# Kernel tuning notes

Measured on AMD Instinct MI355X. Metric: run time of the kernel, lower is better.

## Reference

```python
import jax, jax.numpy as jnp
import numpy as np
import math

C_Z, C_HID, N_HEADS = 128, 32, 4
B, N = 1, 320
LN_EPS = 1e-5


def setup_inputs() -> dict:
    key = jax.random.key(0)
    ks = jax.random.split(key, 9)
    d = C_HID * N_HEADS  # 128
    glorot = math.sqrt(2.0 / (C_Z + d))
    return {
        "z": jax.random.normal(ks[0], (B, N, N, C_Z), jnp.float32),
        "mask_bias": jax.random.normal(ks[1], (B, N, 1, 1, N), jnp.float32),
        "edge_bias": jax.random.normal(ks[2], (B, 1, N_HEADS, N, N), jnp.float32),
        "wq": jax.random.normal(ks[3], (d, C_Z), jnp.float32) * glorot,
        "wk": jax.random.normal(ks[4], (d, C_Z), jnp.float32) * glorot,
        "wv": jax.random.normal(ks[5], (d, C_Z), jnp.float32) * glorot,
        "wg": jax.random.normal(ks[6], (d, C_Z), jnp.float32) * 0.02,
        "wo": jax.random.normal(ks[7], (C_Z, d), jnp.float32) * 0.02,
        "ln_w": jnp.ones((C_Z,), jnp.float32),
        "ln_b": jnp.zeros((C_Z,), jnp.float32),
    }


def reference(z, mask_bias, edge_bias, wq, wk, wv, wg, wo, ln_w, ln_b):
    # LayerNorm over c_z
    mu = jnp.mean(z, axis=-1, keepdims=True)
    var = jnp.mean(jnp.square(z - mu), axis=-1, keepdims=True)
    zn = (z - mu) * jax.lax.rsqrt(var + LN_EPS) * ln_w + ln_b  # [B,I,J,c_z]

    def proj(w):
        p = jnp.einsum("bijd,ed->bije", zn, w)  # [B,I,J,H*c]
        p = p.reshape(zn.shape[:-1] + (N_HEADS, C_HID))  # [B,I,J,H,c]
        return jnp.swapaxes(p, -3, -2)  # [B,I,H,J,c]

    q = proj(wq) / math.sqrt(C_HID)
    k = proj(wk)
    v = proj(wv)

    # scores: [B,I,H,Q,K] + mask_bias [B,I,1,1,K] + edge_bias [B,1,H,Q,K]
    scores = jnp.einsum("bihqc,bihkc->bihqk", q, k) + mask_bias + edge_bias
    a = jax.nn.softmax(scores, axis=-1)
    o = jnp.einsum("bihqk,bihkc->bihqc", a, v)  # [B,I,H,J,c]
    o = jnp.swapaxes(o, -3, -2)  # [B,I,J,H,c]

    g = jax.nn.sigmoid(jnp.einsum("bijd,ed->bije", zn, wg))
    g = g.reshape(zn.shape[:-1] + (N_HEADS, C_HID))
    o = o * g

    o = o.reshape(o.shape[:-2] + (N_HEADS * C_HID,))  # [B,I,J,H*c]
    return jnp.einsum("bije,de->bijd", o, wo)  # [B,I,J,c_z]
```

## Files before the change

### kernel.cpp

```cpp
#include <hip/hip_runtime.h>
#include <hip/hip_bf16.h>

#define NRES 320
#define CZ 128
#define NH 4
#define CH 32
#define DM 128
#define NPOS (NRES*NRES)
#define LN_EPS 1e-5f
#define QSCALE 0.17677669529663687f
#define LOG2E 1.4426950408889634f

using bf16 = __hip_bfloat16;
typedef __attribute__((ext_vector_type(8))) short short8;
typedef __attribute__((ext_vector_type(4))) float floatx4;

__device__ __forceinline__ float bflo(uint32_t u){ return __uint_as_float(u << 16); }
__device__ __forceinline__ float bfhi(uint32_t u){ return __uint_as_float(u & 0xffff0000u); }
__device__ __forceinline__ bf16 tob(float f){ return __float2bfloat16(f); }
__device__ __forceinline__ uint32_t cvtpk(float a, float b){
    uint32_t r;
    asm("v_cvt_pk_bf16_f32 %0, %1, %2" : "=v"(r) : "v"(a), "v"(b));
    return r;
}

__global__ __launch_bounds__(256)
void k_packw(const float* __restrict__ wq, const float* __restrict__ wk,
             const float* __restrict__ wv, const float* __restrict__ wg,
             bf16* __restrict__ Apkh, bf16* __restrict__ Apkl)
{
    const int idx = blockIdx.x * 256 + threadIdx.x;
    const int j = idx & 7, lane = (idx >> 3) & 63;
    const int ks = (idx >> 9) & 3, mf = (idx >> 11) & 3, wid = idx >> 13;
    const int e = wid*64 + mf*16 + (lane & 15);
    const int k = ks*32 + (lane >> 4)*8 + j;
    const float* w = (e >> 7) == 0 ? wq : (e >> 7) == 1 ? wk : (e >> 7) == 2 ? wv : wg;
    float wv_ = w[(e & 127)*CZ + k];
    if (e < 128) wv_ *= QSCALE * LOG2E;
    const bf16 hb = tob(wv_);
    Apkh[idx] = hb;
    Apkl[idx] = tob(wv_ - __bfloat162float(hb));
}

__global__ __launch_bounds__(256)
void k_packwo(const float* __restrict__ wo, bf16* __restrict__ B2h,
              bf16* __restrict__ B2l)
{
    const int idx = blockIdx.x * 256 + threadIdx.x;
    const int j = idx & 7, lane = (idx >> 3) & 63;
    const int nr = (idx >> 9) & 3, ks = (idx >> 11) & 3, wn = idx >> 13;
    const int n = wn*64 + nr*16 + (lane & 15);
    const int k = ks*32 + ((lane >> 4) << 3) + j;
    const float wv_ = wo[n*DM + k];
    const bf16 hb = tob(wv_);
    B2h[idx] = hb;
    B2l[idx] = tob(wv_ - __bfloat162float(hb));
}

__global__ __launch_bounds__(256)
void k_packeb(const float* __restrict__ eb, bf16* __restrict__ ebpk)
{
    const int idx = blockIdx.x * 256 + threadIdx.x;
    const int e = idx & 7;
    const int lane = (idx >> 3) & 63;
    const int nf = (idx >> 9) & 3;
    const int w = (idx >> 11) % 5;
    const int t = (idx / 10240) % 10;
    const int h = idx / 102400;
    const int q = w*64 + nf*16 + (lane & 15);
    const int k = t*32 + (e >> 2)*16 + (lane >> 4)*4 + (e & 3);
    ebpk[idx] = tob(eb[((size_t)h*NRES + q)*NRES + k] * LOG2E);
}

__global__ __launch_bounds__(256)
void k_packmb(const float* __restrict__ mb, float* __restrict__ mbpk)
{
    const int idx = blockIdx.x * 256 + threadIdx.x;
    mbpk[idx] = mb[idx] * LOG2E;
}

__global__ __launch_bounds__(512, 3)
void k_lnproj(const float* __restrict__ z, const float* __restrict__ ln_w,
              const float* __restrict__ ln_b, const bf16* __restrict__ Apkh,
              const bf16* __restrict__ Apkl,
              bf16* __restrict__ qws, bf16* __restrict__ kws,
              bf16* __restrict__ vtws, bf16* __restrict__ gows)
{
    __shared__ __align__(16) char Bsh[16 * 1040];
    __shared__ __align__(16) char Bsl[16 * 1040];
    const int tid = threadIdx.x;
    const int p0 = blockIdx.x * 64;
    const int lane = tid & 63, wid = tid >> 6;
    const int l15 = lane & 15, g = lane >> 4;

    {
        const int r = tid >> 3, t = tid & 7, c0 = t*16;
        const float* zp = z + (size_t)(p0 + r)*CZ + c0;
        float v[16];
        {
            float4 t0 = *(const float4*)(zp + 0);
            float4 t1 = *(const float4*)(zp + 4);
            float4 t2 = *(const float4*)(zp + 8);
            float4 t3 = *(const float4*)(zp + 12);
            v[0]=t0.x; v[1]=t0.y; v[2]=t0.z; v[3]=t0.w;
            v[4]=t1.x; v[5]=t1.y; v[6]=t1.z; v[7]=t1.w;
            v[8]=t2.x; v[9]=t2.y; v[10]=t2.z; v[11]=t2.w;
            v[12]=t3.x; v[13]=t3.y; v[14]=t3.z; v[15]=t3.w;
        }
        float s = 0.f, s2 = 0.f;
        #pragma unroll
        for (int c = 0; c < 16; ++c) { s += v[c]; s2 = fmaf(v[c], v[c], s2); }
        s  += __shfl_xor(s, 1);  s  += __shfl_xor(s, 2);  s  += __shfl_xor(s, 4);
        s2 += __shfl_xor(s2, 1); s2 += __shfl_xor(s2, 2); s2 += __shfl_xor(s2, 4);
        const float mu = s * 0.0078125f;
        const float rs = rsqrtf(s2 * 0.0078125f - mu*mu + LN_EPS);
        float vn[16];
        #pragma unroll
        for (int c = 0; c < 16; ++c)
            vn[c] = (v[c] - mu) * rs * ln_w[c0 + c] + ln_b[c0 + c];
        uint32_t hd[8], ld[8];
        #pragma unroll
        for (int c2 = 0; c2 < 8; ++c2) {
            hd[c2] = cvtpk(vn[2*c2], vn[2*c2+1]);
            ld[c2] = cvtpk(vn[2*c2]   - bflo(hd[c2]),
                           vn[2*c2+1] - bfhi(hd[c2]));
        }
        *(uint4*)(Bsh + (2*t    )*1040 + r*16) = make_uint4(hd[0], hd[1], hd[2], hd[3]);
        *(uint4*)(Bsh + (2*t + 1)*1040 + r*16) = make_uint4(hd[4], hd[5], hd[6], hd[7]);
        *(uint4*)(Bsl + (2*t    )*1040 + r*16) = make_uint4(ld[0], ld[1], ld[2], ld[3]);
        *(uint4*)(Bsl + (2*t + 1)*1040 + r*16) = make_uint4(ld[4], ld[5], ld[6], ld[7]);
    }
    __syncthreads();

    floatx4 acc[4][4];
    #pragma unroll
    for (int mf = 0; mf < 4; ++mf)
        #pragma unroll
        for (int nf = 0; nf < 4; ++nf)
            acc[mf][nf] = (floatx4){0.f, 0.f, 0.f, 0.f};

    const uint4* aph = (const uint4*)Apkh;
    const uint4* apl = (const uint4*)Apkl;
    #pragma unroll
    for (int ks = 0; ks < 4; ++ks) {
        uint4 ahv[4], alv[4];
        #pragma unroll
        for (int mf = 0; mf < 4; ++mf) {
            ahv[mf] = aph[((wid*4 + mf)*4 + ks)*64 + lane];
            alv[mf] = apl[((wid*4 + mf)*4 + ks)*64 + lane];
        }
        #pragma unroll
        for (int nf = 0; nf < 4; ++nf) {
            const int off = (ks*4 + g)*1040 + (16*nf + l15)*16;
            const short8 bh = *(const short8*)(Bsh + off);
            const short8 bl = *(const short8*)(Bsl + off);
            #pragma unroll
            for (int mf = 0; mf < 4; ++mf) {
                const short8 ah = *(const short8*)&ahv[mf];
                const short8 al = *(const short8*)&alv[mf];
                acc[mf][nf] = __builtin_amdgcn_mfma_f32_16x16x32_bf16(ah, bh, acc[mf][nf], 0, 0, 0);
                acc[mf][nf] = __builtin_amdgcn_mfma_f32_16x16x32_bf16(al, bh, acc[mf][nf], 0, 0, 0);
                acc[mf][nf] = __builtin_amdgcn_mfma_f32_16x16x32_bf16(ah, bl, acc[mf][nf], 0, 0, 0);
            }
        }
    }

    const int i = p0 / NRES;
    const int j0 = p0 % NRES;
    #pragma unroll
    for (int mf = 0; mf < 4; ++mf) {
        const int e0 = wid*64 + mf*16 + 4*g;
        const int hh = (e0 >> 5) & 3, c0 = e0 & 31;
        #pragma unroll
        for (int nf = 0; nf < 4; ++nf) {
            const int jl = nf*16 + l15;
            const floatx4 a = acc[mf][nf];
            if (wid < 4) {
                uint2 dw;
                dw.x = cvtpk(a[0], a[1]);
                dw.y = cvtpk(a[2], a[3]);
                bf16* dst = (wid < 2) ? qws : kws;
                const size_t hidx = ((size_t)((i*NH + hh)*NRES) + (j0 + jl))*CH + c0;
                *(uint2*)(dst + hidx) = dw;
            } else if (wid < 6) {
                const size_t vbase = ((size_t)((i*NH + hh)*CH) + c0)*NRES + (j0 + jl);
                vtws[vbase         ] = tob(a[0]);
                vtws[vbase +   NRES] = tob(a[1]);
                vtws[vbase + 2*NRES] = tob(a[2]);
                vtws[vbase + 3*NRES] = tob(a[3]);
            } else {
                const float g0 = 1.f / (1.f + __expf(-a[0]));
                const float g1 = 1.f / (1.f + __expf(-a[1]));
                const float g2 = 1.f / (1.f + __expf(-a[2]));
                const float g3 = 1.f / (1.f + __expf(-a[3]));
                uint2 dw;
                dw.x = cvtpk(g0, g1);
                dw.y = cvtpk(g2, g3);
                *(uint2*)(gows + (size_t)(p0 + jl)*DM + (e0 & 127)) = dw;
            }
        }
    }
}

__global__ __launch_bounds__(320, 3)
void k_attn(const bf16* __restrict__ qws, const bf16* __restrict__ kws,
            const bf16* __restrict__ vtws, bf16* __restrict__ gows,
            const float* __restrict__ mbpk, const bf16* __restrict__ ebpk)
{
    __shared__ __align__(16) char psmem[5 * 64 * 80];
    const int i = blockIdx.x, h = blockIdx.y;
    const int tid = threadIdx.x;
    const int lane = tid & 63, w = tid >> 6;
    const int l15 = lane & 15, g = lane >> 4;
    const size_t slab = (size_t)(i*NH + h) * NRES * CH;
    char* psb = psmem + w*5120;

    const uint4* qg = (const uint4*)(qws + slab);
    const uint4* kg = (const uint4*)(kws + slab);
    const uint4* vg = (const uint4*)(vtws + slab);
    const float* mbr = mbpk + (size_t)i*NRES;
    const uint4* ebp = (const uint4*)ebpk;
    const int ebbase = h*12800 + w*256 + lane;

    short8 bq[4];
    #pragma unroll
    for (int nf = 0; nf < 4; ++nf) {
        uint4 t = qg[(64*w + 16*nf + l15)*4 + g];
        bq[nf] = *(short8*)&t;
    }
    uint4 kc0 = kg[(     l15)*4 + g];
    uint4 kc1 = kg[(16 + l15)*4 + g];
    uint4 ebc[4];
    #pragma unroll
    for (int nf = 0; nf < 4; ++nf) ebc[nf] = ebp[ebbase + nf*64];

    floatx4 o[2][4];
    #pragma unroll
    for (int ma = 0; ma < 2; ++ma)
        #pragma unroll
        for (int nf = 0; nf < 4; ++nf)
            o[ma][nf] = (floatx4){0.f, 0.f, 0.f, 0.f};
    float m[4] = {-1e30f, -1e30f, -1e30f, -1e30f};
    float l[4] = {0.f, 0.f, 0.f, 0.f};

    for (int t = 0; t < 10; ++t) {
        uint4 av0u = vg[(     l15)*40 + 4*t + g];
        uint4 av1u = vg[(16 + l15)*40 + 4*t + g];
        float2 mbv[2][2];
        #pragma unroll
        for (int mi = 0; mi < 2; ++mi)
            #pragma unroll
            for (int rp = 0; rp < 2; ++rp)
                mbv[mi][rp] = *(const float2*)(mbr + 32*t + 16*mi + 4*g + 2*rp);

        const short8 ak0 = *(short8*)&kc0;
        const short8 ak1 = *(short8*)&kc1;
        floatx4 sa[2][4];
        #pragma unroll
        for (int nf = 0; nf < 4; ++nf) {
            sa[0][nf] = __builtin_amdgcn_mfma_f32_16x16x32_bf16(ak0, bq[nf], (floatx4){0.f,0.f,0.f,0.f}, 0, 0, 0);
            sa[1][nf] = __builtin_amdgcn_mfma_f32_16x16x32_bf16(ak1, bq[nf], (floatx4){0.f,0.f,0.f,0.f}, 0, 0, 0);
        }
        const int tn = (t < 9) ? t + 1 : 9;
        uint4 kn0 = kg[(32*tn +      l15)*4 + g];
        uint4 kn1 = kg[(32*tn + 16 + l15)*4 + g];
        uint4 ebn[4];
        #pragma unroll
        for (int nf = 0; nf < 4; ++nf) ebn[nf] = ebp[ebbase + tn*1280 + nf*64];

        float sv[4][2][4];
        float lmax[4];
        #pragma unroll
        for (int nf = 0; nf < 4; ++nf) {
            const uint4 E = ebc[nf];
            sv[nf][0][0] = sa[0][nf][0] + (bflo(E.x) + mbv[0][0].x);
            sv[nf][0][1] = sa[0][nf][1] + (bfhi(E.x) + mbv[0][0].y);
            sv[nf][0][2] = sa[0][nf][2] + (bflo(E.y) + mbv[0][1].x);
            sv[nf][0][3] = sa[0][nf][3] + (bfhi(E.y) + mbv[0][1].y);
            sv[nf][1][0] = sa[1][nf][0] + (bflo(E.z) + mbv[1][0].x);
            sv[nf][1][1] = sa[1][nf][1] + (bfhi(E.z) + mbv[1][0].y);
            sv[nf][1][2] = sa[1][nf][2] + (bflo(E.w) + mbv[1][1].x);
            sv[nf][1][3] = sa[1][nf][3] + (bfhi(E.w) + mbv[1][1].y);
            const float a0 = fmaxf(fmaxf(sv[nf][0][0], sv[nf][0][1]), fmaxf(sv[nf][0][2], sv[nf][0][3]));
            const float a1 = fmaxf(fmaxf(sv[nf][1][0], sv[nf][1][1]), fmaxf(sv[nf][1][2], sv[nf][1][3]));
            lmax[nf] = fmaxf(a0, a1);
        }
        const float gm = fmaxf(fmaxf(lmax[0] - m[0], lmax[1] - m[1]),
                               fmaxf(lmax[2] - m[2], lmax[3] - m[3]));
        if (__any(gm > 12.0f)) {
            #pragma unroll
            for (int nf = 0; nf < 4; ++nf) {
                float pm = lmax[nf];
                pm = fmaxf(pm, __shfl_xor(pm, 16));
                pm = fmaxf(pm, __shfl_xor(pm, 32));
                const float mn = fmaxf(m[nf], pm);
                const float sc = exp2f(m[nf] - mn);
                l[nf] *= sc;
                #pragma unroll
                for (int ma = 0; ma < 2; ++ma)
                    #pragma unroll
                    for (int r = 0; r < 4; ++r)
                        o[ma][nf][r] *= sc;
                m[nf] = mn;
            }
        }
        #pragma unroll
        for (int nf = 0; nf < 4; ++nf) {
            const int qrow = 16*nf + l15;
            #pragma unroll
            for (int mi = 0; mi < 2; ++mi) {
                const float p0 = exp2f(sv[nf][mi][0] - m[nf]);
                const float p1 = exp2f(sv[nf][mi][1] - m[nf]);
                const float p2 = exp2f(sv[nf][mi][2] - m[nf]);
                const float p3 = exp2f(sv[nf][mi][3] - m[nf]);
                l[nf] += (p0 + p1) + (p2 + p3);
                *(uint2*)(psb + qrow*80 + 32*mi + 8*g) =
                    make_uint2(cvtpk(p0, p1), cvtpk(p2, p3));
            }
        }
        const short8 av0 = *(short8*)&av0u;
        const short8 av1 = *(short8*)&av1u;
        #pragma unroll
        for (int nf = 0; nf < 4; ++nf) {
            const short8 bp = *(const short8*)(psb + (16*nf + l15)*80 + 16*g);
            o[0][nf] = __builtin_amdgcn_mfma_f32_16x16x32_bf16(av0, bp, o[0][nf], 0, 0, 0);
            o[1][nf] = __builtin_amdgcn_mfma_f32_16x16x32_bf16(av1, bp, o[1][nf], 0, 0, 0);
        }
        kc0 = kn0; kc1 = kn1;
        #pragma unroll
        for (int nf = 0; nf < 4; ++nf) ebc[nf] = ebn[nf];
    }

    float linv[4];
    #pragma unroll
    for (int nf = 0; nf < 4; ++nf) {
        float ls = l[nf];
        ls += __shfl_xor(ls, 16);
        ls += __shfl_xor(ls, 32);
        linv[nf] = 1.f / ls;
    }
    uint32_t* gp = (uint32_t*)gows;
    #pragma unroll
    for (int nf = 0; nf < 4; ++nf) {
        const int jq = 64*w + 16*nf + l15;
        #pragma unroll
        for (int ma = 0; ma < 2; ++ma)
            #pragma unroll
            for (int rp = 0; rp < 2; ++rp) {
                const size_t idx = ((size_t)(i*NRES + jq))*64 + h*16 + 8*ma + 2*g + rp;
                const uint32_t u = gp[idx];
                const float v0 = o[ma][nf][2*rp    ] * linv[nf] * bflo(u);
                const float v1 = o[ma][nf][2*rp + 1] * linv[nf] * bfhi(u);
                gp[idx] = cvtpk(v0, v1);
            }
    }
}

__global__ __launch_bounds__(512)
void k_outproj(const bf16* __restrict__ gows, const bf16* __restrict__ B2h,
               const bf16* __restrict__ B2l, float* __restrict__ out)
{
    __shared__ __align__(16) char As[16 * 4112];
    const int tid = threadIdx.x;
    const int p0 = blockIdx.x * 256;
    const int lane = tid & 63, wid = tid >> 6;
    const int wm = wid >> 1, wn = wid & 1;

    short8 bh[4][4];
    {
        const uint4* bp = (const uint4*)B2h;
        #pragma unroll
        for (int ks = 0; ks < 4; ++ks)
            #pragma unroll
            for (int nr = 0; nr < 4; ++nr) {
                uint4 t = bp[(((wn*4 + ks)*4) + nr)*64 + lane];
                bh[ks][nr] = *(short8*)&t;
            }
    }

    {
        const uint4* src = (const uint4*)(gows + (size_t)p0 * DM);
        #pragma unroll
        for (int it = 0; it < 8; ++it) {
            const int t = tid + it*512;
            uint4 u = src[t];
            *(uint4*)(As + (t & 15)*4112 + (t >> 4)*16) = u;
        }
    }
    __syncthreads();

    floatx4 acc[4][4];
    #pragma unroll
    for (int m = 0; m < 4; ++m)
        #pragma unroll
        for (int n = 0; n < 4; ++n)
            acc[m][n] = (floatx4){0.f, 0.f, 0.f, 0.f};

    const uint4* bpl = (const uint4*)B2l;
    #pragma unroll
    for (int ks = 0; ks < 4; ++ks) {
        short8 a[4];
        #pragma unroll
        for (int m = 0; m < 4; ++m) {
            const int row = wm*64 + m*16 + (lane & 15);
            a[m] = *(const short8*)(As + (ks*4 + (lane >> 4))*4112 + row*16);
        }
        #pragma unroll
        for (int nr = 0; nr < 4; ++nr) {
            uint4 tl = bpl[(((wn*4 + ks)*4) + nr)*64 + lane];
            const short8 bl = *(short8*)&tl;
            #pragma unroll
            for (int m = 0; m < 4; ++m)
                acc[m][nr] = __builtin_amdgcn_mfma_f32_16x16x32_bf16(a[m], bh[ks][nr], acc[m][nr], 0, 0, 0);
            #pragma unroll
            for (int m = 0; m < 4; ++m)
                acc[m][nr] = __builtin_amdgcn_mfma_f32_16x16x32_bf16(a[m], bl, acc[m][nr], 0, 0, 0);
        }
    }

    #pragma unroll
    for (int m = 0; m < 4; ++m) {
        #pragma unroll
        for (int n = 0; n < 4; ++n) {
            const int d = wn*64 + n*16 + (lane & 15);
            #pragma unroll
            for (int r = 0; r < 4; ++r) {
                const int prow = p0 + wm*64 + m*16 + ((lane >> 4) << 2) + r;
                out[(size_t)prow*DM + d] = acc[m][n][r];
            }
        }
    }
}

extern "C" void kernel_launch(void* const* d_in, const int* in_sizes, int n_in,
                              void* d_out, int out_size, void* d_ws, size_t ws_size,
                              hipStream_t stream)
{
    const float* z   = (const float*)d_in[0];
    const float* mb  = (const float*)d_in[1];
    const float* eb  = (const float*)d_in[2];
    const float* wq  = (const float*)d_in[3];
    const float* wk  = (const float*)d_in[4];
    const float* wv  = (const float*)d_in[5];
    const float* wg  = (const float*)d_in[6];
    const float* wo  = (const float*)d_in[7];
    const float* lnw = (const float*)d_in[8];
    const float* lnb = (const float*)d_in[9];
    float* out = (float*)d_out;

    const size_t SEG = (size_t)NPOS * DM;
    bf16* qws  = (bf16*)d_ws;
    bf16* kws  = qws + SEG;
    bf16* vtws = kws + SEG;
    bf16* gows = vtws + SEG;
    bf16* Apkh = gows + SEG;
    bf16* Apkl = Apkh + 65536;
    bf16* B2h  = Apkl + 65536;
    bf16* B2l  = B2h + 16384;
    bf16* ebpk = B2l + 16384;
    float* mbpk = (float*)(ebpk + 409600);

    k_packw<<<256, 256, 0, stream>>>(wq, wk, wv, wg, Apkh, Apkl);
    k_packwo<<<64, 256, 0, stream>>>(wo, B2h, B2l);
    k_packeb<<<1600, 256, 0, stream>>>(eb, ebpk);
    k_packmb<<<400, 256, 0, stream>>>(mb, mbpk);
    k_lnproj<<<NPOS/64, 512, 0, stream>>>(z, lnw, lnb, Apkh, Apkl, qws, kws, vtws, gows);
    k_attn<<<dim3(NRES, NH), 320, 0, stream>>>(qws, kws, vtws, gows, mbpk, ebpk);
    k_outproj<<<NPOS/256, 512, 0, stream>>>(gows, B2h, B2l, out);
}
```

Before: 166.3 us.

## Fold edge bias into MFMA accumulator and compute row sums via MFMA

Edge bias is now packed as fp32 in the MFMA accumulator layout and passed as the C operand of the QK^T MFMA, which removes the per-element bf16 unpack and add. The softmax denominator is no longer accumulated with scalar adds; an extra MFMA against a ones-vector A operand produces the row sums alongside P·V. In exchange, the edge-bias buffer doubles in size and its loads are no longer prefetched one tile ahead. The kernel also issues one extra MFMA per nf per tile, and the rescale path must scale the added accumulator.

```diff
diff --git a/kernel.cpp b/kernel.cpp
--- a/kernel.cpp
+++ b/kernel.cpp
@@ -58,18 +58,18 @@
 }
 
 __global__ __launch_bounds__(256)
-void k_packeb(const float* __restrict__ eb, bf16* __restrict__ ebpk)
+void k_packeb(const float* __restrict__ eb, float* __restrict__ ebpk)
 {
     const int idx = blockIdx.x * 256 + threadIdx.x;
-    const int e = idx & 7;
-    const int lane = (idx >> 3) & 63;
-    const int nf = (idx >> 9) & 3;
-    const int w = (idx >> 11) % 5;
+    const int r = idx & 3;
+    const int lane = (idx >> 2) & 63;
+    const int mi = (idx >> 8) & 1;
+    const int flat = (idx >> 9) % 20;
     const int t = (idx / 10240) % 10;
     const int h = idx / 102400;
-    const int q = w*64 + nf*16 + (lane & 15);
-    const int k = t*32 + (e >> 2)*16 + (lane >> 4)*4 + (e & 3);
-    ebpk[idx] = tob(eb[((size_t)h*NRES + q)*NRES + k] * LOG2E);
+    const int q = flat*16 + (lane & 15);
+    const int k = t*32 + mi*16 + (lane >> 4)*4 + r;
+    ebpk[idx] = eb[((size_t)h*NRES + q)*NRES + k] * LOG2E;
 }
 
 __global__ __launch_bounds__(256)
@@ -205,7 +205,7 @@
 __global__ __launch_bounds__(320, 3)
 void k_attn(const bf16* __restrict__ qws, const bf16* __restrict__ kws,
             const bf16* __restrict__ vtws, bf16* __restrict__ gows,
-            const float* __restrict__ mbpk, const bf16* __restrict__ ebpk)
+            const float* __restrict__ mbpk, const float* __restrict__ ebpk)
 {
     __shared__ __align__(16) char psmem[5 * 64 * 80];
     const int i = blockIdx.x, h = blockIdx.y;
@@ -219,8 +219,12 @@
     const uint4* kg = (const uint4*)(kws + slab);
     const uint4* vg = (const uint4*)(vtws + slab);
     const float* mbr = mbpk + (size_t)i*NRES;
-    const uint4* ebp = (const uint4*)ebpk;
-    const int ebbase = h*12800 + w*256 + lane;
+    const floatx4* ebp = (const floatx4*)ebpk;
+    const int ebbase = (h*10*20 + 4*w)*2*64 + lane;
+
+    const uint32_t onep = (l15 == 0) ? 0x3F803F80u : 0u;
+    uint4 au = make_uint4(onep, onep, onep, onep);
+    const short8 av2 = *(short8*)&au;
 
     short8 bq[4];
     #pragma unroll
@@ -230,20 +234,24 @@
     }
     uint4 kc0 = kg[(     l15)*4 + g];
     uint4 kc1 = kg[(16 + l15)*4 + g];
-    uint4 ebc[4];
-    #pragma unroll
-    for (int nf = 0; nf < 4; ++nf) ebc[nf] = ebp[ebbase + nf*64];
 
     floatx4 o[2][4];
-    #pragma unroll
-    for (int ma = 0; ma < 2; ++ma)
-        #pragma unroll
-        for (int nf = 0; nf < 4; ++nf)
-            o[ma][nf] = (floatx4){0.f, 0.f, 0.f, 0.f};
+    floatx4 o2[4];
+    #pragma unroll
+    for (int nf = 0; nf < 4; ++nf) {
+        o[0][nf] = (floatx4){0.f, 0.f, 0.f, 0.f};
+        o[1][nf] = (floatx4){0.f, 0.f, 0.f, 0.f};
+        o2[nf]   = (floatx4){0.f, 0.f, 0.f, 0.f};
+    }
     float m[4] = {-1e30f, -1e30f, -1e30f, -1e30f};
-    float l[4] = {0.f, 0.f, 0.f, 0.f};
 
     for (int t = 0; t < 10; ++t) {
+        floatx4 e0[4], e1[4];
+        #pragma unroll
+        for (int nf = 0; nf < 4; ++nf) {
+            e0[nf] = ebp[ebbase + t*2560 + nf*128];
+            e1[nf] = ebp[ebbase + t*2560 + nf*128 + 64];
+        }
         uint4 av0u = vg[(     l15)*40 + 4*t + g];
         uint4 av1u = vg[(16 + l15)*40 + 4*t + g];
         float2 mbv[2][2];
@@ -258,29 +266,25 @@
         floatx4 sa[2][4];
         #pragma unroll
         for (int nf = 0; nf < 4; ++nf) {
-            sa[0][nf] = __builtin_amdgcn_mfma_f32_16x16x32_bf16(ak0, bq[nf], (floatx4){0.f,0.f,0.f,0.f}, 0, 0, 0);
-            sa[1][nf] = __builtin_amdgcn_mfma_f32_16x16x32_bf16(ak1, bq[nf], (floatx4){0.f,0.f,0.f,0.f}, 0, 0, 0);
+            sa[0][nf] = __builtin_amdgcn_mfma_f32_16x16x32_bf16(ak0, bq[nf], e0[nf], 0, 0, 0);
+            sa[1][nf] = __builtin_amdgcn_mfma_f32_16x16x32_bf16(ak1, bq[nf], e1[nf], 0, 0, 0);
         }
         const int tn = (t < 9) ? t + 1 : 9;
         uint4 kn0 = kg[(32*tn +      l15)*4 + g];
         uint4 kn1 = kg[(32*tn + 16 + l15)*4 + g];
-        uint4 ebn[4];
-        #pragma unroll
-        for (int nf = 0; nf < 4; ++nf) ebn[nf] = ebp[ebbase + tn*1280 + nf*64];
 
         float sv[4][2][4];
         float lmax[4];
         #pragma unroll
         for (int nf = 0; nf < 4; ++nf) {
-            const uint4 E = ebc[nf];
-            sv[nf][0][0] = sa[0][nf][0] + (bflo(E.x) + mbv[0][0].x);
-            sv[nf][0][1] = sa[0][nf][1] + (bfhi(E.x) + mbv[0][0].y);
-            sv[nf][0][2] = sa[0][nf][2] + (bflo(E.y) + mbv[0][1].x);
-            sv[nf][0][3] = sa[0][nf][3] + (bfhi(E.y) + mbv[0][1].y);
-            sv[nf][1][0] = sa[1][nf][0] + (bflo(E.z) + mbv[1][0].x);
-            sv[nf][1][1] = sa[1][nf][1] + (bfhi(E.z) + mbv[1][0].y);
-            sv[nf][1][2] = sa[1][nf][2] + (bflo(E.w) + mbv[1][1].x);
-            sv[nf][1][3] = sa[1][nf][3] + (bfhi(E.w) + mbv[1][1].y);
+            sv[nf][0][0] = sa[0][nf][0] + mbv[0][0].x;
+            sv[nf][0][1] = sa[0][nf][1] + mbv[0][0].y;
+            sv[nf][0][2] = sa[0][nf][2] + mbv[0][1].x;
+            sv[nf][0][3] = sa[0][nf][3] + mbv[0][1].y;
+            sv[nf][1][0] = sa[1][nf][0] + mbv[1][0].x;
+            sv[nf][1][1] = sa[1][nf][1] + mbv[1][0].y;
+            sv[nf][1][2] = sa[1][nf][2] + mbv[1][1].x;
+            sv[nf][1][3] = sa[1][nf][3] + mbv[1][1].y;
             const float a0 = fmaxf(fmaxf(sv[nf][0][0], sv[nf][0][1]), fmaxf(sv[nf][0][2], sv[nf][0][3]));
             const float a1 = fmaxf(fmaxf(sv[nf][1][0], sv[nf][1][1]), fmaxf(sv[nf][1][2], sv[nf][1][3]));
             lmax[nf] = fmaxf(a0, a1);
@@ -295,12 +299,14 @@
                 pm = fmaxf(pm, __shfl_xor(pm, 32));
                 const float mn = fmaxf(m[nf], pm);
                 const float sc = exp2f(m[nf] - mn);
-                l[nf] *= sc;
                 #pragma unroll
                 for (int ma = 0; ma < 2; ++ma)
                     #pragma unroll
                     for (int r = 0; r < 4; ++r)
                         o[ma][nf][r] *= sc;
+                #pragma unroll
+                for (int r = 0; r < 4; ++r)
+                    o2[nf][r] *= sc;
                 m[nf] = mn;
             }
         }
@@ -313,7 +319,6 @@
                 const float p1 = exp2f(sv[nf][mi][1] - m[nf]);
                 const float p2 = exp2f(sv[nf][mi][2] - m[nf]);
                 const float p3 = exp2f(sv[nf][mi][3] - m[nf]);
-                l[nf] += (p0 + p1) + (p2 + p3);
                 *(uint2*)(psb + qrow*80 + 32*mi + 8*g) =
                     make_uint2(cvtpk(p0, p1), cvtpk(p2, p3));
             }
@@ -325,18 +330,15 @@
             const short8 bp = *(const short8*)(psb + (16*nf + l15)*80 + 16*g);
             o[0][nf] = __builtin_amdgcn_mfma_f32_16x16x32_bf16(av0, bp, o[0][nf], 0, 0, 0);
             o[1][nf] = __builtin_amdgcn_mfma_f32_16x16x32_bf16(av1, bp, o[1][nf], 0, 0, 0);
+            o2[nf]   = __builtin_amdgcn_mfma_f32_16x16x32_bf16(av2, bp, o2[nf],   0, 0, 0);
         }
         kc0 = kn0; kc1 = kn1;
-        #pragma unroll
-        for (int nf = 0; nf < 4; ++nf) ebc[nf] = ebn[nf];
     }
 
     float linv[4];
     #pragma unroll
     for (int nf = 0; nf < 4; ++nf) {
-        float ls = l[nf];
-        ls += __shfl_xor(ls, 16);
-        ls += __shfl_xor(ls, 32);
+        const float ls = __shfl(o2[nf][0], l15);
         linv[nf] = 1.f / ls;
     }
     uint32_t* gp = (uint32_t*)gows;
@@ -457,8 +459,8 @@
     bf16* Apkl = Apkh + 65536;
     bf16* B2h  = Apkl + 65536;
     bf16* B2l  = B2h + 16384;
-    bf16* ebpk = B2l + 16384;
-    float* mbpk = (float*)(ebpk + 409600);
+    float* ebpk = (float*)(B2l + 16384);
+    float* mbpk = ebpk + 409600;
 
     k_packw<<<256, 256, 0, stream>>>(wq, wk, wv, wg, Apkh, Apkl);
     k_packwo<<<64, 256, 0, stream>>>(wo, B2h, B2l);
```

Measured after the change: 178.0 us. 7.0% more time.

## Split attention into one-wave blocks, fold edge bias and row sums into MFMA

Applied to the files above, without the earlier changes.

The attention kernel now launches one 64-thread block per query chunk instead of five waves per block, giving finer-grained scheduling. The edge bias is fed as the MFMA accumulator input instead of being added afterward. The softmax denominator is computed with an extra MFMA against a ones vector rather than scalar adds and shuffles. This trades extra MFMA work and a higher block count for fewer VALU operations; each block still loads K and V on its own.

```diff
diff --git a/kernel.cpp b/kernel.cpp
--- a/kernel.cpp
+++ b/kernel.cpp
@@ -202,18 +202,16 @@
     }
 }
 
-__global__ __launch_bounds__(320, 3)
+__global__ __launch_bounds__(64, 4)
 void k_attn(const bf16* __restrict__ qws, const bf16* __restrict__ kws,
             const bf16* __restrict__ vtws, bf16* __restrict__ gows,
             const float* __restrict__ mbpk, const bf16* __restrict__ ebpk)
 {
-    __shared__ __align__(16) char psmem[5 * 64 * 80];
-    const int i = blockIdx.x, h = blockIdx.y;
-    const int tid = threadIdx.x;
-    const int lane = tid & 63, w = tid >> 6;
+    __shared__ __align__(16) char psb[64 * 80];
+    const int w = blockIdx.x, i = blockIdx.y, h = blockIdx.z;
+    const int lane = threadIdx.x;
     const int l15 = lane & 15, g = lane >> 4;
     const size_t slab = (size_t)(i*NH + h) * NRES * CH;
-    char* psb = psmem + w*5120;
 
     const uint4* qg = (const uint4*)(qws + slab);
     const uint4* kg = (const uint4*)(kws + slab);
@@ -222,6 +220,10 @@
     const uint4* ebp = (const uint4*)ebpk;
     const int ebbase = h*12800 + w*256 + lane;
 
+    const uint32_t onep = (l15 == 0) ? 0x3F803F80u : 0u;
+    uint4 au = make_uint4(onep, onep, onep, onep);
+    const short8 av2 = *(short8*)&au;
+
     short8 bq[4];
     #pragma unroll
     for (int nf = 0; nf < 4; ++nf) {
@@ -235,52 +237,55 @@
     for (int nf = 0; nf < 4; ++nf) ebc[nf] = ebp[ebbase + nf*64];
 
     floatx4 o[2][4];
-    #pragma unroll
-    for (int ma = 0; ma < 2; ++ma)
-        #pragma unroll
-        for (int nf = 0; nf < 4; ++nf)
-            o[ma][nf] = (floatx4){0.f, 0.f, 0.f, 0.f};
+    floatx4 o2[4];
+    #pragma unroll
+    for (int nf = 0; nf < 4; ++nf) {
+        o[0][nf] = (floatx4){0.f, 0.f, 0.f, 0.f};
+        o[1][nf] = (floatx4){0.f, 0.f, 0.f, 0.f};
+        o2[nf]   = (floatx4){0.f, 0.f, 0.f, 0.f};
+    }
     float m[4] = {-1e30f, -1e30f, -1e30f, -1e30f};
-    float l[4] = {0.f, 0.f, 0.f, 0.f};
 
     for (int t = 0; t < 10; ++t) {
-        uint4 av0u = vg[(     l15)*40 + 4*t + g];
-        uint4 av1u = vg[(16 + l15)*40 + 4*t + g];
-        float2 mbv[2][2];
-        #pragma unroll
-        for (int mi = 0; mi < 2; ++mi)
-            #pragma unroll
-            for (int rp = 0; rp < 2; ++rp)
-                mbv[mi][rp] = *(const float2*)(mbr + 32*t + 16*mi + 4*g + 2*rp);
-
-        const short8 ak0 = *(short8*)&kc0;
-        const short8 ak1 = *(short8*)&kc1;
-        floatx4 sa[2][4];
-        #pragma unroll
-        for (int nf = 0; nf < 4; ++nf) {
-            sa[0][nf] = __builtin_amdgcn_mfma_f32_16x16x32_bf16(ak0, bq[nf], (floatx4){0.f,0.f,0.f,0.f}, 0, 0, 0);
-            sa[1][nf] = __builtin_amdgcn_mfma_f32_16x16x32_bf16(ak1, bq[nf], (floatx4){0.f,0.f,0.f,0.f}, 0, 0, 0);
-        }
         const int tn = (t < 9) ? t + 1 : 9;
         uint4 kn0 = kg[(32*tn +      l15)*4 + g];
         uint4 kn1 = kg[(32*tn + 16 + l15)*4 + g];
         uint4 ebn[4];
         #pragma unroll
         for (int nf = 0; nf < 4; ++nf) ebn[nf] = ebp[ebbase + tn*1280 + nf*64];
+        uint4 av0u = vg[(     l15)*40 + 4*t + g];
+        uint4 av1u = vg[(16 + l15)*40 + 4*t + g];
+        float2 mbv[2][2];
+        #pragma unroll
+        for (int mi = 0; mi < 2; ++mi)
+            #pragma unroll
+            for (int rp = 0; rp < 2; ++rp)
+                mbv[mi][rp] = *(const float2*)(mbr + 32*t + 16*mi + 4*g + 2*rp);
+
+        const short8 ak0 = *(short8*)&kc0;
+        const short8 ak1 = *(short8*)&kc1;
+        floatx4 sa[2][4];
+        #pragma unroll
+        for (int nf = 0; nf < 4; ++nf) {
+            const uint4 E = ebc[nf];
+            const floatx4 c0 = (floatx4){bflo(E.x), bfhi(E.x), bflo(E.y), bfhi(E.y)};
+            const floatx4 c1 = (floatx4){bflo(E.z), bfhi(E.z), bflo(E.w), bfhi(E.w)};
+            sa[0][nf] = __builtin_amdgcn_mfma_f32_16x16x32_bf16(ak0, bq[nf], c0, 0, 0, 0);
+            sa[1][nf] = __builtin_amdgcn_mfma_f32_16x16x32_bf16(ak1, bq[nf], c1, 0, 0, 0);
+        }
 
         float sv[4][2][4];
         float lmax[4];
         #pragma unroll
         for (int nf = 0; nf < 4; ++nf) {
-            const uint4 E = ebc[nf];
-            sv[nf][0][0] = sa[0][nf][0] + (bflo(E.x) + mbv[0][0].x);
-            sv[nf][0][1] = sa[0][nf][1] + (bfhi(E.x) + mbv[0][0].y);
-            sv[nf][0][2] = sa[0][nf][2] + (bflo(E.y) + mbv[0][1].x);
-            sv[nf][0][3] = sa[0][nf][3] + (bfhi(E.y) + mbv[0][1].y);
-            sv[nf][1][0] = sa[1][nf][0] + (bflo(E.z) + mbv[1][0].x);
-            sv[nf][1][1] = sa[1][nf][1] + (bfhi(E.z) + mbv[1][0].y);
-            sv[nf][1][2] = sa[1][nf][2] + (bflo(E.w) + mbv[1][1].x);
-            sv[nf][1][3] = sa[1][nf][3] + (bfhi(E.w) + mbv[1][1].y);
+            sv[nf][0][0] = sa[0][nf][0] + mbv[0][0].x;
+            sv[nf][0][1] = sa[0][nf][1] + mbv[0][0].y;
+            sv[nf][0][2] = sa[0][nf][2] + mbv[0][1].x;
+            sv[nf][0][3] = sa[0][nf][3] + mbv[0][1].y;
+            sv[nf][1][0] = sa[1][nf][0] + mbv[1][0].x;
+            sv[nf][1][1] = sa[1][nf][1] + mbv[1][0].y;
+            sv[nf][1][2] = sa[1][nf][2] + mbv[1][1].x;
+            sv[nf][1][3] = sa[1][nf][3] + mbv[1][1].y;
             const float a0 = fmaxf(fmaxf(sv[nf][0][0], sv[nf][0][1]), fmaxf(sv[nf][0][2], sv[nf][0][3]));
             const float a1 = fmaxf(fmaxf(sv[nf][1][0], sv[nf][1][1]), fmaxf(sv[nf][1][2], sv[nf][1][3]));
             lmax[nf] = fmaxf(a0, a1);
@@ -295,12 +300,14 @@
                 pm = fmaxf(pm, __shfl_xor(pm, 32));
                 const float mn = fmaxf(m[nf], pm);
                 const float sc = exp2f(m[nf] - mn);
-                l[nf] *= sc;
                 #pragma unroll
                 for (int ma = 0; ma < 2; ++ma)
                     #pragma unroll
                     for (int r = 0; r < 4; ++r)
                         o[ma][nf][r] *= sc;
+                #pragma unroll
+                for (int r = 0; r < 4; ++r)
+                    o2[nf][r] *= sc;
                 m[nf] = mn;
             }
         }
@@ -313,7 +320,6 @@
                 const float p1 = exp2f(sv[nf][mi][1] - m[nf]);
                 const float p2 = exp2f(sv[nf][mi][2] - m[nf]);
                 const float p3 = exp2f(sv[nf][mi][3] - m[nf]);
-                l[nf] += (p0 + p1) + (p2 + p3);
                 *(uint2*)(psb + qrow*80 + 32*mi + 8*g) =
                     make_uint2(cvtpk(p0, p1), cvtpk(p2, p3));
             }
@@ -325,6 +331,7 @@
             const short8 bp = *(const short8*)(psb + (16*nf + l15)*80 + 16*g);
             o[0][nf] = __builtin_amdgcn_mfma_f32_16x16x32_bf16(av0, bp, o[0][nf], 0, 0, 0);
             o[1][nf] = __builtin_amdgcn_mfma_f32_16x16x32_bf16(av1, bp, o[1][nf], 0, 0, 0);
+            o2[nf]   = __builtin_amdgcn_mfma_f32_16x16x32_bf16(av2, bp, o2[nf],   0, 0, 0);
         }
         kc0 = kn0; kc1 = kn1;
         #pragma unroll
@@ -334,9 +341,7 @@
     float linv[4];
     #pragma unroll
     for (int nf = 0; nf < 4; ++nf) {
-        float ls = l[nf];
-        ls += __shfl_xor(ls, 16);
-        ls += __shfl_xor(ls, 32);
+        const float ls = __shfl(o2[nf][0], l15);
         linv[nf] = 1.f / ls;
     }
     uint32_t* gp = (uint32_t*)gows;
@@ -465,6 +470,6 @@
     k_packeb<<<1600, 256, 0, stream>>>(eb, ebpk);
     k_packmb<<<400, 256, 0, stream>>>(mb, mbpk);
     k_lnproj<<<NPOS/64, 512, 0, stream>>>(z, lnw, lnb, Apkh, Apkl, qws, kws, vtws, gows);
-    k_attn<<<dim3(NRES, NH), 320, 0, stream>>>(qws, kws, vtws, gows, mbpk, ebpk);
+    k_attn<<<dim3(5, NRES, NH), 64, 0, stream>>>(qws, kws, vtws, gows, mbpk, ebpk);
     k_outproj<<<NPOS/256, 512, 0, stream>>>(gows, B2h, B2l, out);
 }
```

Measured after the change: 237.5 us. 42.8% more time.
